# Performance work log

Measured on AMD Instinct MI355X. Metric: run time of the kernel, lower is better.

## Reference

```python
import jax, jax.numpy as jnp
import numpy as np

OFFSET = 1  # self.offset

def setup_inputs() -> dict:
    key = jax.random.key(0)
    k1, k2, k3, k4, k5 = jax.random.split(key, 5)
    B, D, T, S, N = 16, 512, 1024, 12, 10
    x = jax.random.normal(k1, (B, D, T), dtype=jnp.float32)
    y = jax.random.normal(k2, (B, D, T), dtype=jnp.float32)
    W = jax.random.normal(k3, (D, D, S), dtype=jnp.float32) * 0.05  # ConvTranspose2d weight [in, out, 1, steps] squeezed
    b = jax.random.normal(k4, (D,), dtype=jnp.float32) * 0.05
    neg_idxs = jax.random.randint(k5, (B, N * T), 0, T)
    return {"x": x, "y": y, "W": W, "b": b, "neg_idxs": neg_idxs}


def reference(x, y, W, b, neg_idxs):
    B, F, T = y.shape
    N = neg_idxs.shape[1] // T
    # --- sample_negatives: gather by computed index over flattened y ---
    y_flat = jnp.transpose(y, (1, 0, 2)).reshape(F, B * T)          # [F, B*T]
    idx = (neg_idxs + jnp.arange(B, dtype=neg_idxs.dtype)[:, None] * T).reshape(-1)
    negs = y_flat[:, idx].reshape(F, B, N, T).transpose(2, 1, 0, 3)  # [N, B, F, T]
    targets = jnp.concatenate([y[None], negs], axis=0)               # [C=N+1, B, F, T]
    # --- project_to_steps: ConvTranspose2d with kernel (1, steps) == per-step linear ---
    xp = jnp.einsum('bit,ios->bots', x, W) + b[None, :, None, None]  # [B, F, T, S]
    C = N + 1
    S = xp.shape[-1]
    steps = min(S, T - OFFSET)
    preds, labels = [], []
    for i in range(steps):  # small fixed loop over prediction steps
        off = i + OFFSET
        # [C, B, T-off]: dot over feature dim, copies broadcast over x
        p = jnp.einsum('bft,cbft->cbt', xp[:, :, :T - off, i], targets[:, :, :, off:])
        preds.append(p.reshape(-1))
        lab = jnp.zeros((C, B * (T - off)), dtype=xp.dtype).at[0].set(1.0)
        labels.append(lab.reshape(-1))
    predictions = jnp.concatenate(preds)
    labels_out = jnp.concatenate(labels)
    return predictions, labels_out
```

## Files before the change

kernel.cpp:

```cpp
#include <hip/hip_runtime.h>

typedef __bf16 bf16x8 __attribute__((ext_vector_type(8)));
typedef __bf16 bf16x2 __attribute__((ext_vector_type(2)));
typedef float f32x4 __attribute__((ext_vector_type(4)));

#define B_ 16
#define T_ 1024
#define D_ 512
#define S_ 12
#define C_ 11
static constexpr int P_TOTAL = 2148960;

__device__ __host__ inline constexpr int pred_base(int i) {
  return C_ * B_ * (T_ * i - (i * (i + 1)) / 2);
}

__device__ inline unsigned short f2bf(float f) {
  unsigned int u = __float_as_uint(f);
  u += 0x7FFF + ((u >> 16) & 1);
  return (unsigned short)(u >> 16);
}

__device__ inline int perm5(int v) { return ((v & 15) << 1) | (v >> 4); }

__device__ inline void gld16(const void* g, void* l) {
  __builtin_amdgcn_global_load_lds(
      (const __attribute__((address_space(1))) void*)g,
      (__attribute__((address_space(3))) void*)l, 16, 0, 0);
}

__global__ __launch_bounds__(256) void prep_w(const float* __restrict__ W,
                                              unsigned short* __restrict__ wt) {
  __shared__ unsigned short tile[32][33][12];
  const int i0 = blockIdx.x * 32, o0 = blockIdx.y * 32;
#pragma unroll
  for (int q = 0; q < 48; ++q) {
    int idx = threadIdx.x + q * 256;
    int ii = idx / 384, rem = idx % 384;
    tile[ii][rem / 12][rem % 12] =
        f2bf(W[(size_t)(i0 + ii) * 6144 + (size_t)o0 * 12 + rem]);
  }
  __syncthreads();
#pragma unroll
  for (int q = 0; q < 48; ++q) {
    int idx = threadIdx.x + q * 256;
    int ss = idx / 1024, rem = idx % 1024;
    int oo = rem / 32, ii = rem % 32;
    wt[(size_t)ss * (D_ * D_) + (size_t)(o0 + oo) * D_ + i0 + perm5(ii)] =
        tile[ii][oo][ss];
  }
}

__global__ __launch_bounds__(256) void prep_t2(const float* __restrict__ xin,
                                               const float* __restrict__ yin,
                                               unsigned short* __restrict__ xo,
                                               unsigned short* __restrict__ yo) {
  __shared__ float tile[32][33];
  const int t0 = blockIdx.x * 32;
  const int d0 = blockIdx.y * 32;
  const int b = blockIdx.z & 15;
  const float* in = (blockIdx.z < 16) ? xin : yin;
  unsigned short* ob = (blockIdx.z < 16) ? xo : yo;
  const float* ib = in + (size_t)b * D_ * T_;
  const int r = threadIdx.x / 32, c = threadIdx.x % 32;
#pragma unroll
  for (int p = 0; p < 4; ++p) {
    int rr = r + p * 8;
    tile[rr][c] = ib[(size_t)(d0 + rr) * T_ + t0 + c];
  }
  __syncthreads();
  unsigned short* op = ob + (size_t)b * T_ * D_;
#pragma unroll
  for (int p = 0; p < 4; ++p) {
    int rr = r + p * 8;
    op[(size_t)(t0 + rr) * D_ + d0 + perm5(c)] = f2bf(tile[c][rr]);
  }
}

__global__ __launch_bounds__(512, 1) void gemm_xp(
    const unsigned short* __restrict__ xb,
    const unsigned short* __restrict__ wt,
    const float* __restrict__ bias,
    unsigned short* __restrict__ xp,
    int tiles, int mtiles) {
  __shared__ char ldsb[131072];
  const int tid = threadIdx.x;
  const int w = tid >> 6, l = tid & 63;
  const int gm = w >> 2, gn = w & 3;
  const int fr = l & 15, sgrp = l >> 4;

  const int dox0 = tid * 16, dox1 = tid * 16 + 8192;
  const int rl0 = dox0 >> 7, rl1 = dox1 >> 7;
  const int col = dox0 & 127;
  const int sco0 = rl0 * 1024 + (col ^ ((rl0 & 7) << 4));
  const int sco1 = rl1 * 1024 + (col ^ ((rl1 & 7) << 4));

  auto stageH = [&](const char* panel, int ks, int half, int ldsBase) {
    const char* s = panel + half * 131072 + ks * 128;
    char* d = ldsb + ldsBase + half * 16384;
    gld16(s + sco0, d + dox0);
    gld16(s + sco1, d + dox1);
  };

  const int sw = (fr & 7) << 4;
  const int colk0 = (sgrp * 16) ^ sw;
  const int colk1 = (64 + sgrp * 16) ^ sw;
  const int aRowB = (gm * 64 + fr) * 128;
  const int bRowB = 32768 + (gn * 32 + fr) * 128;

  auto ldf = [&](int off) -> bf16x8 {
    return *(const bf16x8*)(ldsb + off);
  };

  auto decode = [&](int t, const unsigned short*& Ag, const unsigned short*& Bg,
                    int& n0v, int& miv, int& siv) {
    miv = t % mtiles;
    int rest = t / mtiles;
    int ni = rest & 1;
    siv = rest >> 1;
    Ag = xb + (size_t)(miv * 256) * D_;
    Bg = wt + ((size_t)siv * D_ + ni * 256) * D_;
    n0v = ni * 256;
  };

  int ti = blockIdx.x;
  if (ti >= tiles) return;
  const unsigned short *Ag, *Bg, *Agn = nullptr, *Bgn = nullptr;
  int n0, mi, si, n0n, min_, sin_;
  decode(ti, Ag, Bg, n0, mi, si);
  int tin = ti + gridDim.x;
  bool hasNext = tin < tiles;
  if (hasNext) decode(tin, Agn, Bgn, n0n, min_, sin_);

#define BAR()  asm volatile("" ::: "memory"); __builtin_amdgcn_s_barrier(); \
               asm volatile("" ::: "memory")

  stageH((const char*)Ag, 0, 0, 0);
  stageH((const char*)Bg, 0, 0, 32768);
  stageH((const char*)Ag, 0, 1, 0);
  stageH((const char*)Bg, 0, 1, 32768);
  asm volatile("s_waitcnt vmcnt(4)" ::: "memory");
  BAR();

  while (true) {
    f32x4 acc[8][4];
#pragma unroll
    for (int a = 0; a < 8; ++a)
#pragma unroll
      for (int bq = 0; bq < 4; ++bq)
#pragma unroll
        for (int e = 0; e < 4; ++e) acc[a][bq][e] = 0.f;

    float bv[2][2];
#pragma unroll
    for (int nh = 0; nh < 2; ++nh)
#pragma unroll
      for (int fn = 0; fn < 2; ++fn)
        bv[nh][fn] = bias[n0 + gn * 32 + nh * 128 + fn * 16 + fr];

#pragma unroll
    for (int ks = 0; ks < 8; ++ks) {
      const int bufB = (ks & 1) * 65536;
      const int nbufB = bufB ^ 65536;
      const bool st = (ks < 7) || hasNext;
      const char* pA = (ks < 7) ? (const char*)Ag : (const char*)Agn;
      const char* pB = (ks < 7) ? (const char*)Bg : (const char*)Bgn;
      const int kn = (ks < 7) ? ks + 1 : 0;
      bf16x8 af[2][4], b0[2][2], b1[2][2];

#pragma unroll
      for (int fm = 0; fm < 4; ++fm) {
        af[0][fm] = ldf(bufB + aRowB + fm * 2048 + colk0);
        af[1][fm] = ldf(bufB + aRowB + fm * 2048 + colk1);
      }
#pragma unroll
      for (int fn = 0; fn < 2; ++fn) {
        b0[0][fn] = ldf(bufB + bRowB + fn * 2048 + colk0);
        b0[1][fn] = ldf(bufB + bRowB + fn * 2048 + colk1);
      }
      if (st) {
        stageH(pA, kn, 0, nbufB);
        asm volatile("s_waitcnt vmcnt(2)" ::: "memory");
      } else {
        asm volatile("s_waitcnt vmcnt(0)" ::: "memory");
      }
      BAR();
      __builtin_amdgcn_s_setprio(1);
#pragma unroll
      for (int kk = 0; kk < 2; ++kk)
#pragma unroll
        for (int fm = 0; fm < 4; ++fm)
#pragma unroll
          for (int fn = 0; fn < 2; ++fn)
            acc[fm][fn] = __builtin_amdgcn_mfma_f32_16x16x32_bf16(
                af[kk][fm], b0[kk][fn], acc[fm][fn], 0, 0, 0);
      __builtin_amdgcn_s_setprio(0);
      BAR();

#pragma unroll
      for (int fn = 0; fn < 2; ++fn) {
        b1[0][fn] = ldf(bufB + bRowB + 16384 + fn * 2048 + colk0);
        b1[1][fn] = ldf(bufB + bRowB + 16384 + fn * 2048 + colk1);
      }
      if (st) stageH(pB, kn, 0, nbufB + 32768);
      BAR();
      __builtin_amdgcn_s_setprio(1);
#pragma unroll
      for (int kk = 0; kk < 2; ++kk)
#pragma unroll
        for (int fm = 0; fm < 4; ++fm)
#pragma unroll
          for (int fn = 0; fn < 2; ++fn)
            acc[fm][2 + fn] = __builtin_amdgcn_mfma_f32_16x16x32_bf16(
                af[kk][fm], b1[kk][fn], acc[fm][2 + fn], 0, 0, 0);
      __builtin_amdgcn_s_setprio(0);
      BAR();

#pragma unroll
      for (int fm = 0; fm < 4; ++fm) {
        af[0][fm] = ldf(bufB + aRowB + 16384 + fm * 2048 + colk0);
        af[1][fm] = ldf(bufB + aRowB + 16384 + fm * 2048 + colk1);
      }
      if (st) stageH(pA, kn, 1, nbufB);
      BAR();
      __builtin_amdgcn_s_setprio(1);
#pragma unroll
      for (int kk = 0; kk < 2; ++kk)
#pragma unroll
        for (int fm = 0; fm < 4; ++fm)
#pragma unroll
          for (int fn = 0; fn < 2; ++fn)
            acc[4 + fm][2 + fn] = __builtin_amdgcn_mfma_f32_16x16x32_bf16(
                af[kk][fm], b1[kk][fn], acc[4 + fm][2 + fn], 0, 0, 0);
      __builtin_amdgcn_s_setprio(0);
      BAR();

      if (st) stageH(pB, kn, 1, nbufB + 32768);
      BAR();
      __builtin_amdgcn_s_setprio(1);
#pragma unroll
      for (int kk = 0; kk < 2; ++kk)
#pragma unroll
        for (int fm = 0; fm < 4; ++fm)
#pragma unroll
          for (int fn = 0; fn < 2; ++fn)
            acc[4 + fm][fn] = __builtin_amdgcn_mfma_f32_16x16x32_bf16(
                af[kk][fm], b0[kk][fn], acc[4 + fm][fn], 0, 0, 0);
      __builtin_amdgcn_s_setprio(0);
      if (st) asm volatile("s_waitcnt vmcnt(4)" ::: "memory");
      BAR();
    }

#pragma unroll
    for (int mh = 0; mh < 2; ++mh) {
#pragma unroll
      for (int fm = 0; fm < 4; ++fm) {
#pragma unroll
        for (int r = 0; r < 4; ++r) {
          int m = mi * 256 + gm * 64 + mh * 128 + fm * 16 + sgrp * 4 + r;
          int bl = m >> 10, t = m & 1023;
          size_t orow = (((size_t)bl * S_ + si) * T_ + t) * D_;
#pragma unroll
          for (int nh = 0; nh < 2; ++nh) {
            bf16x2 pk;
            pk[0] = (__bf16)(acc[mh * 4 + fm][nh * 2 + 0][r] + bv[nh][0]);
            pk[1] = (__bf16)(acc[mh * 4 + fm][nh * 2 + 1][r] + bv[nh][1]);
            int op = n0 + nh * 128 + gn * 32 + 2 * fr;
            *(bf16x2*)(xp + orow + op) = pk;
          }
        }
      }
    }

    if (!hasNext) break;
    ti = tin;
    Ag = Agn; Bg = Bgn; n0 = n0n; mi = min_; si = sin_;
    tin = ti + gridDim.x;
    hasNext = tin < tiles;
    if (hasNext) decode(tin, Agn, Bgn, n0n, min_, sin_);
  }
#undef BAR
}

__global__ __launch_bounds__(256) void pred_k(
    const unsigned short* __restrict__ xp,
    const unsigned short* __restrict__ yT,
    const int* __restrict__ negs,
    float* __restrict__ preds, int b0, int do_labels) {
  const int w = threadIdx.x >> 6, l = threadIdx.x & 63;
  const int bl = blockIdx.y;
  const int b = b0 + bl;
  const int fr = l & 15;
  const int koff = (l >> 4) * 8;

  const unsigned short* arow[2];
  const unsigned short* brow[2];
  int tts[2];
#pragma unroll
  for (int q = 0; q < 2; ++q) {
    int tt = blockIdx.x * 4 + w + q * 512;
    tts[q] = tt;
    int t = tt - 1 - fr;
    bool av = (fr < S_) && (t >= 0);
    arow[q] = xp + (((size_t)bl * S_ + (av ? fr : 0)) * T_ + (av ? t : 0)) * D_;
    int j = tt;
    if (fr >= 1 && fr <= 10) j = negs[b * (10 * T_) + (fr - 1) * T_ + tt];
    brow[q] = yT + ((size_t)b * T_ + j) * D_;
  }

  f32x4 acc[2];
#pragma unroll
  for (int q = 0; q < 2; ++q)
#pragma unroll
    for (int e = 0; e < 4; ++e) acc[q][e] = 0.f;

#pragma unroll
  for (int kk = 0; kk < 16; ++kk) {
#pragma unroll
    for (int q = 0; q < 2; ++q) {
      bf16x8 a = *(const bf16x8*)(arow[q] + kk * 32 + koff);
      bf16x8 bb = *(const bf16x8*)(brow[q] + kk * 32 + koff);
      acc[q] = __builtin_amdgcn_mfma_f32_16x16x32_bf16(a, bb, acc[q], 0, 0, 0);
    }
  }

#pragma unroll
  for (int q = 0; q < 2; ++q) {
#pragma unroll
    for (int r = 0; r < 4; ++r) {
      int ii = (l >> 4) * 4 + r;
      int to = tts[q] - 1 - ii;
      if (ii < S_ && fr < C_ && tts[q] >= 1 && to >= 0) {
        int len = T_ - 1 - ii;
        preds[pred_base(ii) + ((size_t)fr * B_ + b) * len + to] = acc[q][r];
      }
    }
  }

  if (do_labels) {
    float* lab = preds + P_TOTAL;
    const int stride = gridDim.x * gridDim.y * 256;
    int k = (blockIdx.y * gridDim.x + blockIdx.x) * 256 + threadIdx.x;
    for (; k < P_TOTAL; k += stride) {
      int i = 0;
#pragma unroll
      for (int qq = 1; qq < 12; ++qq)
        if (k >= pred_base(qq)) i = qq;
      int rel = k - pred_base(i);
      int len = T_ - 1 - i;
      lab[k] = (rel < B_ * len) ? 1.0f : 0.0f;
    }
  }
}

extern "C" void kernel_launch(void* const* d_in, const int* in_sizes, int n_in,
                              void* d_out, int out_size, void* d_ws, size_t ws_size,
                              hipStream_t stream) {
  (void)in_sizes; (void)n_in; (void)out_size;
  const float* x = (const float*)d_in[0];
  const float* y = (const float*)d_in[1];
  const float* W = (const float*)d_in[2];
  const float* bias = (const float*)d_in[3];
  const int* negs = (const int*)d_in[4];
  float* out = (float*)d_out;
  char* ws = (char*)d_ws;

  unsigned short* wt = (unsigned short*)ws;
  unsigned short* xb = (unsigned short*)(ws + 6291456);
  unsigned short* yT = (unsigned short*)(ws + 6291456 + 16777216);
  unsigned short* xp = (unsigned short*)(ws + 6291456 + 2 * 16777216);
  const size_t fixed = 6291456 + (size_t)2 * 16777216;
  const size_t xp_per_b = (size_t)S_ * T_ * D_ * 2;
  int nb = 1;
  if (ws_size > fixed) {
    size_t cap = (ws_size - fixed) / xp_per_b;
    nb = cap < 1 ? 1 : (cap > 16 ? 16 : (int)cap);
  }

  hipLaunchKernelGGL(prep_w, dim3(16, 16), dim3(256), 0, stream, W, wt);
  hipLaunchKernelGGL(prep_t2, dim3(32, 16, 32), dim3(256), 0, stream, x, y, xb, yT);

  for (int b0 = 0; b0 < B_; b0 += nb) {
    int bc = (B_ - b0) < nb ? (B_ - b0) : nb;
    int tiles = bc * 4 * 2 * 12;
    int grid = tiles < 256 ? tiles : 256;
    hipLaunchKernelGGL(gemm_xp, dim3(grid), dim3(512), 0, stream,
                       xb + (size_t)b0 * T_ * D_, wt, bias, xp,
                       tiles, bc * 4);
    hipLaunchKernelGGL(pred_k, dim3(128, bc), dim3(256), 0, stream,
                       xp, yT, negs, out, b0, (int)(b0 == 0));
  }
}
```

Before: 201.8 us.

## Stage xp rows through swizzled LDS with double-buffered async loads in pred_k

The pred kernel now loads the 12 step rows of xp into per-wave shared memory with direct global-to-LDS loads (gld16). The LDS layout is XOR-swizzled, and the K dimension is processed in four double-buffered quarters with explicit vmcnt/lgkmcnt waits. The aim is to replace scattered per-lane 16-byte A-operand global reads, which included masked lanes, with coalesced loads that overlap the MFMA work. In exchange the kernel uses 48KB of LDS per block, which may lower occupancy, and it depends on hand-placed waitcnts being correct.

```diff
diff --git a/kernel.cpp b/kernel.cpp
--- a/kernel.cpp
+++ b/kernel.cpp
@@ -287,26 +287,47 @@
     const unsigned short* __restrict__ yT,
     const int* __restrict__ negs,
     float* __restrict__ preds, int b0, int do_labels) {
+  __shared__ char plds[49152];
   const int w = threadIdx.x >> 6, l = threadIdx.x & 63;
   const int bl = blockIdx.y;
   const int b = b0 + bl;
   const int fr = l & 15;
-  const int koff = (l >> 4) * 8;
-
-  const unsigned short* arow[2];
+  const int sgrp = l >> 4;
+  const int koff = sgrp * 8;
+  const int r_ld = l >> 4;
+  const int c16 = l & 15;
+
+  int tts[2];
   const unsigned short* brow[2];
-  int tts[2];
+  const char* asrc[2][3];
 #pragma unroll
   for (int q = 0; q < 2; ++q) {
     int tt = blockIdx.x * 4 + w + q * 512;
     tts[q] = tt;
-    int t = tt - 1 - fr;
-    bool av = (fr < S_) && (t >= 0);
-    arow[q] = xp + (((size_t)bl * S_ + (av ? fr : 0)) * T_ + (av ? t : 0)) * D_;
     int j = tt;
     if (fr >= 1 && fr <= 10) j = negs[b * (10 * T_) + (fr - 1) * T_ + tt];
     brow[q] = yT + ((size_t)b * T_ + j) * D_;
-  }
+#pragma unroll
+    for (int i = 0; i < 3; ++i) {
+      int r = i * 4 + r_ld;
+      int t = tt - 1 - r;
+      if (t < 0) t = 0;
+      asrc[q][i] = (const char*)(xp + (((size_t)bl * S_ + r) * T_ + t) * D_)
+                   + ((c16 * 16) ^ ((r & 7) << 4));
+    }
+  }
+  char* pbase = plds + w * 12288;
+
+  auto stageQ = [&](int q, int qu, int buf) {
+#pragma unroll
+    for (int i = 0; i < 3; ++i)
+      gld16(asrc[q][i] + qu * 256,
+            pbase + (q * 2 + buf) * 3072 + i * 1024 + l * 16);
+  };
+
+  const int frc = (fr < S_) ? fr : 0;
+  const int swp = (frc & 7) << 4;
+  const int arow0 = frc * 256;
 
   f32x4 acc[2];
 #pragma unroll
@@ -314,13 +335,30 @@
 #pragma unroll
     for (int e = 0; e < 4; ++e) acc[q][e] = 0.f;
 
-#pragma unroll
-  for (int kk = 0; kk < 16; ++kk) {
-#pragma unroll
-    for (int q = 0; q < 2; ++q) {
-      bf16x8 a = *(const bf16x8*)(arow[q] + kk * 32 + koff);
-      bf16x8 bb = *(const bf16x8*)(brow[q] + kk * 32 + koff);
-      acc[q] = __builtin_amdgcn_mfma_f32_16x16x32_bf16(a, bb, acc[q], 0, 0, 0);
+  stageQ(0, 0, 0);
+  stageQ(1, 0, 0);
+
+#pragma unroll
+  for (int qu = 0; qu < 4; ++qu) {
+    asm volatile("s_waitcnt lgkmcnt(0)" ::: "memory");
+    if (qu < 3) {
+      stageQ(0, qu + 1, (qu + 1) & 1);
+      stageQ(1, qu + 1, (qu + 1) & 1);
+      asm volatile("s_waitcnt vmcnt(6)" ::: "memory");
+    } else {
+      asm volatile("s_waitcnt vmcnt(0)" ::: "memory");
+    }
+#pragma unroll
+    for (int kq = 0; kq < 4; ++kq) {
+      const int kk = qu * 4 + kq;
+      const int acol = (sgrp * 16 + kq * 64) ^ swp;
+#pragma unroll
+      for (int q = 0; q < 2; ++q) {
+        bf16x8 a = *(const bf16x8*)(pbase + (q * 2 + (qu & 1)) * 3072 +
+                                    arow0 + acol);
+        bf16x8 bb = *(const bf16x8*)(brow[q] + kk * 32 + koff);
+        acc[q] = __builtin_amdgcn_mfma_f32_16x16x32_bf16(a, bb, acc[q], 0, 0, 0);
+      }
     }
   }
 
@@ -328,7 +366,7 @@
   for (int q = 0; q < 2; ++q) {
 #pragma unroll
     for (int r = 0; r < 4; ++r) {
-      int ii = (l >> 4) * 4 + r;
+      int ii = sgrp * 4 + r;
       int to = tts[q] - 1 - ii;
       if (ii < S_ && fr < C_ && tts[q] >= 1 && to >= 0) {
         int len = T_ - 1 - ii;
```

After: 194.1 us. -3.8%, faster.
